# Performance work log

Hardware: AMD Instinct MI355X
Metric: run time of the kernel (lower is better)

## Reference

```python
import jax, jax.numpy as jnp
import numpy as np

ITER = 10
ALPHA = 0.5
SMOOTH = 1.0
EPS = 1e-07


def _maxpool2d(x, win, pad):
    # torch F.max_pool2d pads with -inf for max pooling; reduce_window with -inf init matches exactly
    return jax.lax.reduce_window(
        x, -jnp.inf, jax.lax.max,
        (1, 1, win[0], win[1]), (1, 1, 1, 1),
        [(0, 0), (0, 0), (pad[0], pad[0]), (pad[1], pad[1])])


def soft_erode(x):
    p1 = -_maxpool2d(-x, (3, 1), (1, 0))
    p2 = -_maxpool2d(-x, (1, 3), (0, 1))
    return jnp.minimum(p1, p2)


def soft_dilate(x):
    return _maxpool2d(x, (3, 3), (1, 1))


def soft_open(x):
    return soft_dilate(soft_erode(x))


def soft_skel(img, n_iter):
    skel = jax.nn.relu(img - soft_open(img))

    def body(_, carry):
        im, sk = carry
        im = soft_erode(im)
        delta = jax.nn.relu(im - soft_open(im))
        sk = sk + jax.nn.relu(delta - sk * delta)
        return (im, sk)

    _, skel = jax.lax.fori_loop(0, n_iter, body, (img, skel))
    return skel


def _soft_dice(output, target):
    bs = output.shape[0]
    o = output.reshape(bs, 1, -1)  # binary mode: [B,1,N]
    t = target.reshape(bs, 1, -1)
    inter = jnp.sum(o * t, axis=(0, 2))
    card = jnp.sum(o + t, axis=(0, 2))
    score = (2.0 * inter + SMOOTH) / jnp.maximum(card + SMOOTH, EPS)
    loss = (1.0 - score) * (jnp.sum(t, axis=(0, 2)) > 0).astype(score.dtype)
    return loss.mean()


def _soft_cldice(skel_output, skel_target):
    bs = skel_output.shape[0]
    o = skel_output.reshape(bs, 1, -1)
    t = skel_target.reshape(bs, 1, -1)
    tprec = (jnp.sum(o * t, axis=(0, 2)) + SMOOTH) / (jnp.sum(o, axis=(0, 2)) + SMOOTH)
    tsens = (jnp.sum(t * o, axis=(0, 2)) + SMOOTH) / (jnp.sum(t, axis=(0, 2)) + SMOOTH)
    score = 2.0 * (tprec * tsens) / (tprec + tsens)
    loss = (1.0 - score) * (jnp.sum(t, axis=(0, 2)) > 0).astype(score.dtype)
    return loss.mean()


def setup_inputs() -> dict:
    key = jax.random.key(0)
    k1, k2 = jax.random.split(key)
    output = jax.random.normal(k1, (8, 1, 1024, 1024), dtype=jnp.float32)
    target = jax.random.randint(k2, (8, 1, 1024, 1024), 0, 2).astype(jnp.int32)
    return {"output": output, "target": target}


def reference(output, target):
    # binary mode: logsigmoid(x).exp() == sigmoid(x)
    probs = jax.nn.sigmoid(output)
    tgt = target.astype(probs.dtype)
    dice = _soft_dice(probs, tgt)
    skel_o = soft_skel(probs, ITER)
    skel_t = soft_skel(tgt, ITER)
    cl_dice = _soft_cldice(skel_o, skel_t)
    return (1.0 - ALPHA) * dice + ALPHA * cl_dice
```

## Files before the change

kernel.cpp:

```cpp
#include <hip/hip_runtime.h>
#include <math.h>


#define HH 1024
#define WW 1024
#define BATCH 8
#define HW (HH * WW)
#define NITER 10
#define TW 128
#define TH 64
#define AH 88
#define CXC 20
#define NCELL (AH * CXC)
#define BMP 6
#define NQO 440
#define NT 1024
#define NBX 8
#define NBY 16
#define NBLK (NBX * NBY * BATCH)

typedef _Float16 h8 __attribute__((ext_vector_type(8)));
typedef unsigned int u32;
typedef unsigned long long u64;
typedef u32 u4v __attribute__((ext_vector_type(4)));

#define MIN2(a, b) __builtin_elementwise_min(a, b)
#define MAX2(a, b) __builtin_elementwise_max(a, b)

__device__ __forceinline__ u32 alignb(u32 hi, u32 lo) {
    return (u32)((((u64)hi << 32) | lo) >> 16);
}
__device__ __forceinline__ u32 fsh(u32 hi, u32 lo, int s) {
    return (u32)((((u64)hi << 32) | lo) >> s);
}
__device__ __forceinline__ u32 dw0(h8 v) { return __builtin_bit_cast(u4v, v).x; }
__device__ __forceinline__ u32 dw3(h8 v) { return __builtin_bit_cast(u4v, v).w; }
__device__ __forceinline__ h8 shl1(h8 v, u32 l3) {
    u4v d = __builtin_bit_cast(u4v, v);
    u4v r;
    r.x = alignb(d.x, l3); r.y = alignb(d.y, d.x);
    r.z = alignb(d.z, d.y); r.w = alignb(d.w, d.z);
    return __builtin_bit_cast(h8, r);
}
__device__ __forceinline__ h8 shr1(h8 v, u32 r0d) {
    u4v d = __builtin_bit_cast(u4v, v);
    u4v r;
    r.x = alignb(d.y, d.x); r.y = alignb(d.z, d.y);
    r.z = alignb(d.w, d.z); r.w = alignb(r0d, d.w);
    return __builtin_bit_cast(h8, r);
}
__device__ __forceinline__ float sigm(float x) { return 1.0f / (1.0f + __expf(-x)); }
__device__ __forceinline__ int imin(int a, int b) { return a < b ? a : b; }
__device__ __forceinline__ int imax(int a, int b) { return a > b ? a : b; }

__global__ __launch_bounds__(NT) void cldice_mega_kernel(const float* __restrict__ logits,
                                                         const int* __restrict__ target,
                                                         float* __restrict__ partials) {
    __shared__ __align__(16) h8 bufO[2][NCELL];
    __shared__ u32 bmT[2][AH * BMP];
    __shared__ u32 pub[256];
    __shared__ float red[96];

    const int tid = threadIdx.x;
    const int img = blockIdx.z;
    const int x0 = blockIdx.x * TW, y0 = blockIdx.y * TH;

    const _Float16 HIF = (_Float16)__builtin_inff();
    const h8 HI8 = (h8)HIF;
    const h8 LO8 = (h8)(-HIF);
    const h8 Z8 = (h8)(_Float16)0;

    const bool has_e = tid < NQO;
    int e_base = CXC, e_M = 0;
    bool e_rok[4] = {false, false, false, false};
    if (has_e) {
        int q = tid / 20, c = tid - (tid / 20) * 20;
        int r = 1 + 4 * q;
        if (r > 83) r = 83;
        e_base = r * CXC + c;
        int cMx = imin(8 * c + 7, 159 - 8 * c);
#pragma unroll
        for (int k = 0; k < 4; ++k)
            e_M = imax(e_M, imin(imin(r + k, 87 - (r + k)), cMx));
        e_M = imin(e_M, NITER + 1);
        bool colOOB = (x0 == 0 && c < 2) || (x0 == WW - TW && c >= 18);
#pragma unroll
        for (int k = 0; k < 4; ++k)
            e_rok[k] = !colOOB && ((unsigned)(y0 - 12 + r + k) < HH);
    }

    const bool has_o = (tid >= 512) && (tid < 768);
    const int op = tid & 255;
    const int opr = op >> 4, oc = op & 15;
    const int orow = 12 + 4 * opr;
    const int ob = orow * CXC + 2 + oc;
    const bool rT = (y0 == 0 && opr == 0);
    const bool rB = (y0 == HH - TH && opr == 15);
    const bool cL = (x0 == 0 && oc == 0);
    const bool cR = (x0 == WW - TW && oc == 15);

    const bool has_te = (tid >= 768) && (tid < 768 + 22 * BMP);
    int tb = BMP, te_M = 0;
    u32 oobm = 0;
    bool trok[4] = {false, false, false, false};
    if (has_te) {
        int p = tid - 768;
        int q = p / BMP, c = p - (p / BMP) * BMP;
        int r = 1 + 4 * q;
        if (r > 83) r = 83;
        tb = r * BMP + c;
        int pxlo = imax(32 * c - 16, 0), pxhi = imin(32 * c + 15, 159);
        int cMx = imin(pxhi, 159 - pxlo);
#pragma unroll
        for (int k = 0; k < 4; ++k)
            te_M = imax(te_M, imin(imin(r + k, 87 - (r + k)), cMx));
        te_M = imin(te_M, NITER + 1);
        if (c == 0) oobm |= 0x0000FFFFu;
        if (c == 5) oobm |= 0xFFFF0000u;
        if (x0 == 0 && c == 0) oobm = 0xFFFFFFFFu;
        if (x0 == WW - TW && c == 5) oobm = 0xFFFFFFFFu;
#pragma unroll
        for (int k = 0; k < 4; ++k)
            trok[k] = (unsigned)(y0 - 12 + r + k) < HH;
    }

    const bool has_to = tid >= 960;
    const int tp = tid - 960;
    const int topr = (tp >> 2) & 15, td = (tp & 3) + 1;
    const int torow = 12 + 4 * topr;
    const int tob = torow * BMP + td;
    const bool trT = (y0 == 0 && topr == 0);
    const bool trB = (y0 == HH - TH && topr == 15);
    const bool tcL = (x0 == 0 && td == 1);
    const bool tcR = (x0 == WW - TW && td == 4);

    if (tid < AH) {
        unsigned short* p16 = (unsigned short*)bmT[0];
        p16[tid * 12 + 0] = 0xFFFFu;
        p16[tid * 12 + 11] = 0xFFFFu;
        unsigned short* q16 = (unsigned short*)bmT[1];
        q16[tid * 12 + 0] = 0xFFFFu;
        q16[tid * 12 + 11] = 0xFFFFu;
    }

    float d_inter = 0.f, d_card = 0.f, d_st = 0.f;
#pragma unroll
    for (int s = 0; s < 2; ++s) {
        int li = tid + NT * s;
        if (li < NCELL) {
            int r = li / CXC, c = li - (li / CXC) * CXC;
            int gy = y0 - 12 + r, gx = x0 - 16 + 8 * c;
            bool gyok = (unsigned)gy < HH;
            float vo[8];
            u32 tb8 = 0;
            if (gyok && gx >= 0 && gx + 7 < WW) {
                int g = img * HW + gy * WW + gx;
                float4 a = *(const float4*)(logits + g);
                float4 b = *(const float4*)(logits + g + 4);
                vo[0] = sigm(a.x); vo[1] = sigm(a.y); vo[2] = sigm(a.z); vo[3] = sigm(a.w);
                vo[4] = sigm(b.x); vo[5] = sigm(b.y); vo[6] = sigm(b.z); vo[7] = sigm(b.w);
                int4 p = *(const int4*)(target + g);
                int4 q = *(const int4*)(target + g + 4);
                tb8 = (p.x != 0 ? 1u : 0u) | (p.y != 0 ? 2u : 0u) |
                      (p.z != 0 ? 4u : 0u) | (p.w != 0 ? 8u : 0u) |
                      (q.x != 0 ? 16u : 0u) | (q.y != 0 ? 32u : 0u) |
                      (q.z != 0 ? 64u : 0u) | (q.w != 0 ? 128u : 0u);
            } else {
#pragma unroll
                for (int j = 0; j < 8; ++j) {
                    int gxx = gx + j;
                    if (gyok && (unsigned)gxx < WW) {
                        int g = img * HW + gy * WW + gxx;
                        vo[j] = sigm(logits[g]);
                        tb8 |= (target[g] != 0 ? 1u : 0u) << j;
                    } else { vo[j] = INFINITY; tb8 |= 1u << j; }
                }
            }
            h8 ho;
#pragma unroll
            for (int j = 0; j < 8; ++j) ho[j] = (_Float16)vo[j];
            bufO[0][li] = ho;
            ((unsigned char*)bmT[0])[r * 24 + 2 + c] = (unsigned char)tb8;
            if (r >= 12 && r < 76 && c >= 2 && c < 18) {
#pragma unroll
                for (int j = 0; j < 8; ++j) {
                    float t = (float)((tb8 >> j) & 1u);
                    d_inter += t * vo[j];
                    d_card += vo[j] + t;
                    d_st += t;
                }
            }
        }
    }
    __syncthreads();
    h8 imv[4], sk[4];
    if (has_o) {
#pragma unroll
        for (int k = 0; k < 4; ++k) imv[k] = bufO[0][ob + k * CXC];
    }
#pragma unroll
    for (int k = 0; k < 4; ++k) sk[k] = Z8;
    u32 timv[4] = {0, 0, 0, 0}, tsk[4] = {0, 0, 0, 0};
    if (has_to) {
#pragma unroll
        for (int k = 0; k < 4; ++k) timv[k] = bmT[0][tob + k * BMP];
    }

#define PHASE(LV, rdO, wrO, rdT, wrT)                                              \
    {                                                                              \
        const int PL = (LV);                                                       \
                           \
        if (has_e && PL <= e_M) {                                                  \
            const h8* b = (rdO);                                                   \
            h8 u  = b[e_base - CXC];                                               \
            h8 c0 = b[e_base],           c1 = b[e_base + CXC];                     \
            h8 c2 = b[e_base + 2 * CXC], c3 = b[e_base + 3 * CXC];                 \
            h8 d  = b[e_base + 4 * CXC];                                           \
            h8 l0 = b[e_base - 1],           l1 = b[e_base + CXC - 1];             \
            h8 l2 = b[e_base + 2 * CXC - 1], l3 = b[e_base + 3 * CXC - 1];         \
            h8 r0 = b[e_base + 1],           r1 = b[e_base + CXC + 1];             \
            h8 r2 = b[e_base + 2 * CXC + 1], r3 = b[e_base + 3 * CXC + 1];         \
            h8 p01 = MIN2(c0, c1), p12 = MIN2(c1, c2), p23 = MIN2(c2, c3);         \
            h8 v0 = MIN2(u, p01), v1 = MIN2(p01, c2);                              \
            h8 v2 = MIN2(p12, c3), v3 = MIN2(p23, d);                              \
            h8 eo0 = MIN2(v0, MIN2(shl1(c0, dw3(l0)), shr1(c0, dw0(r0))));         \
            h8 eo1 = MIN2(v1, MIN2(shl1(c1, dw3(l1)), shr1(c1, dw0(r1))));         \
            h8 eo2 = MIN2(v2, MIN2(shl1(c2, dw3(l2)), shr1(c2, dw0(r2))));         \
            h8 eo3 = MIN2(v3, MIN2(shl1(c3, dw3(l3)), shr1(c3, dw0(r3))));         \
            (wrO)[e_base]           = e_rok[0] ? eo0 : HI8;                        \
            (wrO)[e_base + CXC]     = e_rok[1] ? eo1 : HI8;                        \
            (wrO)[e_base + 2 * CXC] = e_rok[2] ? eo2 : HI8;                        \
            (wrO)[e_base + 3 * CXC] = e_rok[3] ? eo3 : HI8;                        \
        }                                                                          \
                                              \
        if (has_te && PL <= te_M) {                                                \
            const u32* bt = (rdT);                                                 \
            u32 m0 = bt[tb - BMP], m1 = bt[tb], m2 = bt[tb + BMP];                 \
            u32 m3 = bt[tb + 2 * BMP], m4 = bt[tb + 3 * BMP], m5 = bt[tb + 4 * BMP]; \
            u32 lw0 = bt[tb - 1],           lw1 = bt[tb + BMP - 1];                \
            u32 lw2 = bt[tb + 2 * BMP - 1], lw3 = bt[tb + 3 * BMP - 1];            \
            u32 rw0 = bt[tb + 1],           rw1 = bt[tb + BMP + 1];                \
            u32 rw2 = bt[tb + 2 * BMP + 1], rw3 = bt[tb + 3 * BMP + 1];            \
            u32 p12 = m1 & m2, p23 = m2 & m3, p34 = m3 & m4;                       \
            u32 v0 = m0 & p12, v1 = p12 & m3, v2 = p23 & m4, v3 = p34 & m5;        \
            u32 et0 = v0 & fsh(m1, lw0, 31) & fsh(rw0, m1, 1);                     \
            u32 et1 = v1 & fsh(m2, lw1, 31) & fsh(rw1, m2, 1);                     \
            u32 et2 = v2 & fsh(m3, lw2, 31) & fsh(rw2, m3, 1);                     \
            u32 et3 = v3 & fsh(m4, lw3, 31) & fsh(rw3, m4, 1);                     \
            (wrT)[tb]           = trok[0] ? (et0 | oobm) : 0xFFFFFFFFu;            \
            (wrT)[tb + BMP]     = trok[1] ? (et1 | oobm) : 0xFFFFFFFFu;            \
            (wrT)[tb + 2 * BMP] = trok[2] ? (et2 | oobm) : 0xFFFFFFFFu;            \
            (wrT)[tb + 3 * BMP] = trok[3] ? (et3 | oobm) : 0xFFFFFFFFu;            \
        }                                                                          \
                \
        if (has_o && PL >= 2) {                                                    \
            const h8* b = (rdO);                                                   \
            h8 m0 = b[ob - CXC], m1 = b[ob], m2 = b[ob + CXC];                     \
            h8 m3 = b[ob + 2 * CXC], m4 = b[ob + 3 * CXC], m5 = b[ob + 4 * CXC];  \
            h8 nm0 = m1, nm1 = m2, nm2 = m3, nm3 = m4;                             \
            if (rT) m0 = LO8;                                                      \
            if (rB) m5 = LO8;                                                      \
            h8 q12 = MAX2(m1, m2), q34 = MAX2(m3, m4);                             \
            h8 Mc0 = MAX2(m0, q12), Mc1 = MAX2(q12, m3);                           \
            h8 Mc2 = MAX2(m2, q34), Mc3 = MAX2(q34, m5);                           \
            h8 a0 = b[ob - CXC - 1], a1 = b[ob - 1], a2 = b[ob + CXC - 1];         \
            h8 a3 = b[ob + 2 * CXC - 1], a4 = b[ob + 3 * CXC - 1];                 \
            h8 a5 = b[ob + 4 * CXC - 1];                                           \
            if (rT) a0 = LO8;                                                      \
            if (rB) a5 = LO8;                                                      \
            h8 s12 = MAX2(a1, a2), s34 = MAX2(a3, a4);                             \
            h8 Ml0 = MAX2(a0, s12), Ml1 = MAX2(s12, a3);                           \
            h8 Ml2 = MAX2(a2, s34), Ml3 = MAX2(s34, a5);                           \
            if (cL) { Ml0 = LO8; Ml1 = LO8; Ml2 = LO8; Ml3 = LO8; }                \
            h8 b0 = b[ob - CXC + 1], b1 = b[ob + 1], b2 = b[ob + CXC + 1];         \
            h8 b3 = b[ob + 2 * CXC + 1], b4 = b[ob + 3 * CXC + 1];                 \
            h8 b5 = b[ob + 4 * CXC + 1];                                           \
            if (rT) b0 = LO8;                                                      \
            if (rB) b5 = LO8;                                                      \
            h8 t12 = MAX2(b1, b2), t34 = MAX2(b3, b4);                             \
            h8 Mr0 = MAX2(b0, t12), Mr1 = MAX2(t12, b3);                           \
            h8 Mr2 = MAX2(b2, t34), Mr3 = MAX2(t34, b5);                           \
            if (cR) { Mr0 = LO8; Mr1 = LO8; Mr2 = LO8; Mr3 = LO8; }                \
            h8 o0 = MAX2(Mc0, MAX2(shl1(Mc0, dw3(Ml0)), shr1(Mc0, dw0(Mr0))));     \
            h8 o1 = MAX2(Mc1, MAX2(shl1(Mc1, dw3(Ml1)), shr1(Mc1, dw0(Mr1))));     \
            h8 o2 = MAX2(Mc2, MAX2(shl1(Mc2, dw3(Ml2)), shr1(Mc2, dw0(Mr2))));     \
            h8 o3 = MAX2(Mc3, MAX2(shl1(Mc3, dw3(Ml3)), shr1(Mc3, dw0(Mr3))));     \
            h8 d0 = MAX2(imv[0] - o0, Z8);                                         \
            h8 d1 = MAX2(imv[1] - o1, Z8);                                         \
            h8 d2 = MAX2(imv[2] - o2, Z8);                                         \
            h8 d3 = MAX2(imv[3] - o3, Z8);                                         \
            if (PL == 2) { sk[0] = d0; sk[1] = d1; sk[2] = d2; sk[3] = d3; }       \
            else {                                                                 \
                sk[0] = sk[0] + MAX2(d0 - sk[0] * d0, Z8);                         \
                sk[1] = sk[1] + MAX2(d1 - sk[1] * d1, Z8);                         \
                sk[2] = sk[2] + MAX2(d2 - sk[2] * d2, Z8);                         \
                sk[3] = sk[3] + MAX2(d3 - sk[3] * d3, Z8);                         \
            }                                                                      \
            imv[0] = nm0; imv[1] = nm1; imv[2] = nm2; imv[3] = nm3;                \
        }                                                                          \
                            \
        if (has_to && PL >= 2) {                                                   \
            const u32* bt = (rdT);                                                 \
            u32 m0 = bt[tob - BMP], m1 = bt[tob], m2 = bt[tob + BMP];              \
            u32 m3 = bt[tob + 2 * BMP], m4 = bt[tob + 3 * BMP];                    \
            u32 m5 = bt[tob + 4 * BMP];                                            \
            u32 nm0 = m1, nm1 = m2, nm2 = m3, nm3 = m4;                            \
            u32 l0 = bt[tob - BMP - 1], l1 = bt[tob - 1], l2 = bt[tob + BMP - 1];  \
            u32 l3 = bt[tob + 2 * BMP - 1], l4 = bt[tob + 3 * BMP - 1];            \
            u32 l5 = bt[tob + 4 * BMP - 1];                                        \
            u32 r0 = bt[tob - BMP + 1], r1 = bt[tob + 1], r2 = bt[tob + BMP + 1];  \
            u32 r3 = bt[tob + 2 * BMP + 1], r4 = bt[tob + 3 * BMP + 1];            \
            u32 r5 = bt[tob + 4 * BMP + 1];                                        \
            if (trT) { m0 = 0; l0 = 0; r0 = 0; }                                   \
            if (trB) { m5 = 0; l5 = 0; r5 = 0; }                                   \
            if (tcL) { l0 = 0; l1 = 0; l2 = 0; l3 = 0; l4 = 0; l5 = 0; }           \
            if (tcR) { r0 = 0; r1 = 0; r2 = 0; r3 = 0; r4 = 0; r5 = 0; }           \
            u32 q12 = m1 | m2, q34 = m3 | m4;                                      \
            u32 Vc0 = m0 | q12, Vc1 = q12 | m3, Vc2 = m2 | q34, Vc3 = q34 | m5;    \
            u32 s12 = l1 | l2, s34 = l3 | l4;                                      \
            u32 Vl0 = l0 | s12, Vl1 = s12 | l3, Vl2 = l2 | s34, Vl3 = s34 | l5;    \
            u32 t12 = r1 | r2, t34 = r3 | r4;                                      \
            u32 Vr0 = r0 | t12, Vr1 = t12 | r3, Vr2 = r2 | t34, Vr3 = t34 | r5;    \
            u32 o0 = Vc0 | fsh(Vc0, Vl0, 31) | fsh(Vr0, Vc0, 1);                   \
            u32 o1 = Vc1 | fsh(Vc1, Vl1, 31) | fsh(Vr1, Vc1, 1);                   \
            u32 o2 = Vc2 | fsh(Vc2, Vl2, 31) | fsh(Vr2, Vc2, 1);                   \
            u32 o3 = Vc3 | fsh(Vc3, Vl3, 31) | fsh(Vr3, Vc3, 1);                   \
            tsk[0] |= timv[0] & ~o0;                                               \
            tsk[1] |= timv[1] & ~o1;                                               \
            tsk[2] |= timv[2] & ~o2;                                               \
            tsk[3] |= timv[3] & ~o3;                                               \
            timv[0] = nm0; timv[1] = nm1; timv[2] = nm2; timv[3] = nm3;            \
        }                                                                          \
        __syncthreads();                                                           \
    }

    for (int L = 1; L <= NITER + 2; L += 2) {
        PHASE(L,     bufO[0], bufO[1], bmT[0], bmT[1])
        PHASE(L + 1, bufO[1], bufO[0], bmT[1], bmT[0])
    }
#undef PHASE

    float I = 0.f, So = 0.f, St = 0.f;
    if (has_to) {
#pragma unroll
        for (int k = 0; k < 4; ++k) {
            pub[(tp << 2) + k] = tsk[k];
            St += (float)__popc(tsk[k]);
        }
    }
    __syncthreads();
    if (has_o) {
        int tt = (opr << 2) + (oc >> 2);
        int sh = (oc & 3) * 8;
#pragma unroll
        for (int k = 0; k < 4; ++k) {
            u32 w = pub[(tt << 2) + k] >> sh;
#pragma unroll
            for (int j = 0; j < 8; ++j) {
                float a = (float)sk[k][j];
                So += a;
                if ((w >> j) & 1u) I += a;
            }
        }
    }

    float v6[6] = {d_inter, d_card, d_st, I, So, St};
#pragma unroll
    for (int q = 0; q < 6; ++q)
        for (int off = 32; off > 0; off >>= 1) v6[q] += __shfl_down(v6[q], off);
    int lane = tid & 63, w = tid >> 6;
    if (lane == 0) {
#pragma unroll
        for (int q = 0; q < 6; ++q) red[w * 6 + q] = v6[q];
    }
    __syncthreads();
    if (tid == 0) {
        int bid = (blockIdx.z * gridDim.y + blockIdx.y) * gridDim.x + blockIdx.x;
#pragma unroll
        for (int q = 0; q < 6; ++q) {
            float s = 0.f;
#pragma unroll
            for (int ww = 0; ww < 16; ++ww) s += red[ww * 6 + q];
            partials[q * NBLK + bid] = s;
        }
    }
}

__global__ __launch_bounds__(1024) void final_kernel(const float* __restrict__ partials,
                                                     float* __restrict__ out) {
    float s[6] = {0.f, 0.f, 0.f, 0.f, 0.f, 0.f};
    for (int i = threadIdx.x; i < NBLK; i += 1024) {
#pragma unroll
        for (int q = 0; q < 6; ++q) s[q] += partials[q * NBLK + i];
    }
#pragma unroll
    for (int q = 0; q < 6; ++q)
        for (int off = 32; off > 0; off >>= 1) s[q] += __shfl_down(s[q], off);
    __shared__ float red[96];
    int lane = threadIdx.x & 63, w = threadIdx.x >> 6;
    if (lane == 0) {
#pragma unroll
        for (int q = 0; q < 6; ++q) red[w * 6 + q] = s[q];
    }
    __syncthreads();
    if (threadIdx.x == 0) {
        float t[6];
#pragma unroll
        for (int q = 0; q < 6; ++q) {
            float a = 0.f;
#pragma unroll
            for (int ww = 0; ww < 16; ++ww) a += red[ww * 6 + q];
            t[q] = a;
        }
        float inter = t[0], card = t[1], sumt = t[2];
        float I = t[3], So = t[4], St = t[5];
        float score_d = (2.0f * inter + 1.0f) / fmaxf(card + 1.0f, 1e-7f);
        float dice = (1.0f - score_d) * (sumt > 0.0f ? 1.0f : 0.0f);
        float tprec = (I + 1.0f) / (So + 1.0f);
        float tsens = (I + 1.0f) / (St + 1.0f);
        float score_c = 2.0f * (tprec * tsens) / (tprec + tsens);
        float cl = (1.0f - score_c) * (St > 0.0f ? 1.0f : 0.0f);
        out[0] = 0.5f * dice + 0.5f * cl;
    }
}

extern "C" void kernel_launch(void* const* d_in, const int* in_sizes, int n_in,
                              void* d_out, int out_size, void* d_ws, size_t ws_size,
                              hipStream_t stream) {
    const float* logits = (const float*)d_in[0];
    const int* target = (const int*)d_in[1];
    float* out = (float*)d_out;
    float* partials = (float*)d_ws;

    dim3 grid(NBX, NBY, BATCH);
    cldice_mega_kernel<<<grid, NT, 0, stream>>>(logits, target, partials);
    final_kernel<<<1, 1024, 0, stream>>>(partials, out);
}
```

Before: 169.6 us.

## Pad LDS row pitch and fuse final reduction via last-block atomic counter

```diff
diff --git a/kernel.cpp b/kernel.cpp
--- a/kernel.cpp
+++ b/kernel.cpp
@@ -10,7 +10,8 @@
 #define TW 128
 #define TH 64
 #define AH 88
-#define CXC 20
+#define CXR 20
+#define CXC 21
 #define NCELL (AH * CXC)
 #define BMP 6
 #define NQO 440
@@ -55,7 +56,8 @@
 
 __global__ __launch_bounds__(NT) void cldice_mega_kernel(const float* __restrict__ logits,
                                                          const int* __restrict__ target,
-                                                         float* __restrict__ partials) {
+                                                         float* __restrict__ partials,
+                                                         float* __restrict__ out) {
     __shared__ __align__(16) h8 bufO[2][NCELL];
     __shared__ u32 bmT[2][AH * BMP];
     __shared__ u32 pub[256];
@@ -149,45 +151,50 @@
         int li = tid + NT * s;
         if (li < NCELL) {
             int r = li / CXC, c = li - (li / CXC) * CXC;
-            int gy = y0 - 12 + r, gx = x0 - 16 + 8 * c;
-            bool gyok = (unsigned)gy < HH;
-            float vo[8];
-            u32 tb8 = 0;
-            if (gyok && gx >= 0 && gx + 7 < WW) {
-                int g = img * HW + gy * WW + gx;
-                float4 a = *(const float4*)(logits + g);
-                float4 b = *(const float4*)(logits + g + 4);
-                vo[0] = sigm(a.x); vo[1] = sigm(a.y); vo[2] = sigm(a.z); vo[3] = sigm(a.w);
-                vo[4] = sigm(b.x); vo[5] = sigm(b.y); vo[6] = sigm(b.z); vo[7] = sigm(b.w);
-                int4 p = *(const int4*)(target + g);
-                int4 q = *(const int4*)(target + g + 4);
-                tb8 = (p.x != 0 ? 1u : 0u) | (p.y != 0 ? 2u : 0u) |
-                      (p.z != 0 ? 4u : 0u) | (p.w != 0 ? 8u : 0u) |
-                      (q.x != 0 ? 16u : 0u) | (q.y != 0 ? 32u : 0u) |
-                      (q.z != 0 ? 64u : 0u) | (q.w != 0 ? 128u : 0u);
+            if (c >= CXR) {
+                bufO[0][li] = HI8;
+                bufO[1][li] = HI8;
             } else {
-#pragma unroll
-                for (int j = 0; j < 8; ++j) {
-                    int gxx = gx + j;
-                    if (gyok && (unsigned)gxx < WW) {
-                        int g = img * HW + gy * WW + gxx;
-                        vo[j] = sigm(logits[g]);
-                        tb8 |= (target[g] != 0 ? 1u : 0u) << j;
-                    } else { vo[j] = INFINITY; tb8 |= 1u << j; }
+                int gy = y0 - 12 + r, gx = x0 - 16 + 8 * c;
+                bool gyok = (unsigned)gy < HH;
+                float vo[8];
+                u32 tb8 = 0;
+                if (gyok && gx >= 0 && gx + 7 < WW) {
+                    int g = img * HW + gy * WW + gx;
+                    float4 a = *(const float4*)(logits + g);
+                    float4 b = *(const float4*)(logits + g + 4);
+                    vo[0] = sigm(a.x); vo[1] = sigm(a.y); vo[2] = sigm(a.z); vo[3] = sigm(a.w);
+                    vo[4] = sigm(b.x); vo[5] = sigm(b.y); vo[6] = sigm(b.z); vo[7] = sigm(b.w);
+                    int4 p = *(const int4*)(target + g);
+                    int4 q = *(const int4*)(target + g + 4);
+                    tb8 = (p.x != 0 ? 1u : 0u) | (p.y != 0 ? 2u : 0u) |
+                          (p.z != 0 ? 4u : 0u) | (p.w != 0 ? 8u : 0u) |
+                          (q.x != 0 ? 16u : 0u) | (q.y != 0 ? 32u : 0u) |
+                          (q.z != 0 ? 64u : 0u) | (q.w != 0 ? 128u : 0u);
+                } else {
+#pragma unroll
+                    for (int j = 0; j < 8; ++j) {
+                        int gxx = gx + j;
+                        if (gyok && (unsigned)gxx < WW) {
+                            int g = img * HW + gy * WW + gxx;
+                            vo[j] = sigm(logits[g]);
+                            tb8 |= (target[g] != 0 ? 1u : 0u) << j;
+                        } else { vo[j] = INFINITY; tb8 |= 1u << j; }
+                    }
                 }
-            }
-            h8 ho;
-#pragma unroll
-            for (int j = 0; j < 8; ++j) ho[j] = (_Float16)vo[j];
-            bufO[0][li] = ho;
-            ((unsigned char*)bmT[0])[r * 24 + 2 + c] = (unsigned char)tb8;
-            if (r >= 12 && r < 76 && c >= 2 && c < 18) {
-#pragma unroll
-                for (int j = 0; j < 8; ++j) {
-                    float t = (float)((tb8 >> j) & 1u);
-                    d_inter += t * vo[j];
-                    d_card += vo[j] + t;
-                    d_st += t;
+                h8 ho;
+#pragma unroll
+                for (int j = 0; j < 8; ++j) ho[j] = (_Float16)vo[j];
+                bufO[0][li] = ho;
+                ((unsigned char*)bmT[0])[r * 24 + 2 + c] = (unsigned char)tb8;
+                if (r >= 12 && r < 76 && c >= 2 && c < 18) {
+#pragma unroll
+                    for (int j = 0; j < 8; ++j) {
+                        float t = (float)((tb8 >> j) & 1u);
+                        d_inter += t * vo[j];
+                        d_card += vo[j] + t;
+                        d_st += t;
+                    }
                 }
             }
         }
@@ -374,6 +381,7 @@
         for (int q = 0; q < 6; ++q) red[w * 6 + q] = v6[q];
     }
     __syncthreads();
+    u32* ctr = (u32*)(partials + 6 * NBLK);
     if (tid == 0) {
         int bid = (blockIdx.z * gridDim.y + blockIdx.y) * gridDim.x + blockIdx.x;
 #pragma unroll
@@ -383,44 +391,45 @@
             for (int ww = 0; ww < 16; ++ww) s += red[ww * 6 + q];
             partials[q * NBLK + bid] = s;
         }
-    }
-}
-
-__global__ __launch_bounds__(1024) void final_kernel(const float* __restrict__ partials,
-                                                     float* __restrict__ out) {
-    float s[6] = {0.f, 0.f, 0.f, 0.f, 0.f, 0.f};
-    for (int i = threadIdx.x; i < NBLK; i += 1024) {
-#pragma unroll
-        for (int q = 0; q < 6; ++q) s[q] += partials[q * NBLK + i];
-    }
-#pragma unroll
-    for (int q = 0; q < 6; ++q)
-        for (int off = 32; off > 0; off >>= 1) s[q] += __shfl_down(s[q], off);
-    __shared__ float red[96];
-    int lane = threadIdx.x & 63, w = threadIdx.x >> 6;
-    if (lane == 0) {
-#pragma unroll
-        for (int q = 0; q < 6; ++q) red[w * 6 + q] = s[q];
+        __threadfence();
+        u32 old = atomicAdd(ctr, 1u);
+        pub[0] = (old == (u32)(NBLK - 1)) ? 1u : 0u;
     }
     __syncthreads();
-    if (threadIdx.x == 0) {
-        float t[6];
-#pragma unroll
-        for (int q = 0; q < 6; ++q) {
-            float a = 0.f;
-#pragma unroll
-            for (int ww = 0; ww < 16; ++ww) a += red[ww * 6 + q];
-            t[q] = a;
-        }
-        float inter = t[0], card = t[1], sumt = t[2];
-        float I = t[3], So = t[4], St = t[5];
-        float score_d = (2.0f * inter + 1.0f) / fmaxf(card + 1.0f, 1e-7f);
-        float dice = (1.0f - score_d) * (sumt > 0.0f ? 1.0f : 0.0f);
-        float tprec = (I + 1.0f) / (So + 1.0f);
-        float tsens = (I + 1.0f) / (St + 1.0f);
-        float score_c = 2.0f * (tprec * tsens) / (tprec + tsens);
-        float cl = (1.0f - score_c) * (St > 0.0f ? 1.0f : 0.0f);
-        out[0] = 0.5f * dice + 0.5f * cl;
+    if (pub[0]) {
+        __threadfence();
+        float s6[6] = {0.f, 0.f, 0.f, 0.f, 0.f, 0.f};
+        for (int i = tid; i < NBLK; i += NT) {
+#pragma unroll
+            for (int q = 0; q < 6; ++q) s6[q] += partials[q * NBLK + i];
+        }
+#pragma unroll
+        for (int q = 0; q < 6; ++q)
+            for (int off = 32; off > 0; off >>= 1) s6[q] += __shfl_down(s6[q], off);
+        if (lane == 0) {
+#pragma unroll
+            for (int q = 0; q < 6; ++q) red[w * 6 + q] = s6[q];
+        }
+        __syncthreads();
+        if (tid == 0) {
+            float t[6];
+#pragma unroll
+            for (int q = 0; q < 6; ++q) {
+                float a = 0.f;
+#pragma unroll
+                for (int ww = 0; ww < 16; ++ww) a += red[ww * 6 + q];
+                t[q] = a;
+            }
+            float inter = t[0], card = t[1], sumt = t[2];
+            float Is = t[3], So_ = t[4], St_ = t[5];
+            float score_d = (2.0f * inter + 1.0f) / fmaxf(card + 1.0f, 1e-7f);
+            float dice = (1.0f - score_d) * (sumt > 0.0f ? 1.0f : 0.0f);
+            float tprec = (Is + 1.0f) / (So_ + 1.0f);
+            float tsens = (Is + 1.0f) / (St_ + 1.0f);
+            float score_c = 2.0f * (tprec * tsens) / (tprec + tsens);
+            float cl = (1.0f - score_c) * (St_ > 0.0f ? 1.0f : 0.0f);
+            out[0] = 0.5f * dice + 0.5f * cl;
+        }
     }
 }
 
@@ -432,7 +441,8 @@
     float* out = (float*)d_out;
     float* partials = (float*)d_ws;
 
+    hipMemsetAsync((char*)d_ws + 6 * NBLK * sizeof(float), 0, 4, stream);
+
     dim3 grid(NBX, NBY, BATCH);
-    cldice_mega_kernel<<<grid, NT, 0, stream>>>(logits, target, partials);
-    final_kernel<<<1, 1024, 0, stream>>>(partials, out);
-}
+    cldice_mega_kernel<<<grid, NT, 0, stream>>>(logits, target, partials, out);
+}
```

After: 197.1 us. 16.2% more time.
